# Kernel tuning notes

Measured on AMD Instinct MI355X. Metric: run time of the kernel, lower is better.

Reference implementation:

```python
import jax, jax.numpy as jnp
import numpy as np
import math

L, D, H, DK, DFF, B, S = 4, 512, 8, 256, 2048, 8, 256
HD = H * DK
EPS = 1e-6


def _norm(x, alpha, bias):
    # torch: alpha*(x-mean)/(std_unbiased + eps) + bias  (std uses ddof=1)
    mu = x.mean(axis=-1, keepdims=True)
    var = ((x - mu) ** 2).sum(axis=-1, keepdims=True) / (x.shape[-1] - 1)
    return alpha * (x - mu) / (jnp.sqrt(var) + EPS) + bias


def _positional_encoding():
    pos = jnp.arange(S, dtype=jnp.float32)[:, None]          # [S,1]
    i = jnp.arange(0, D, 2, dtype=jnp.float32)               # even indices
    pe_sin = jnp.sin(pos / (S ** (2.0 * i / D)))             # [S,D/2]
    pe_cos = jnp.cos(pos / (S ** (2.0 * (i + 1.0) / D)))     # [S,D/2]
    pe = jnp.zeros((S, D), dtype=jnp.float32)
    pe = pe.at[:, 0::2].set(pe_sin).at[:, 1::2].set(pe_cos)
    return pe


def setup_inputs() -> dict:
    key = jax.random.key(0)
    ks = jax.random.split(key, 16)
    sc = 0.02
    inp = {
        "data": jax.random.normal(ks[0], (B, S, D), dtype=jnp.float32),
        "attn_m": jax.random.randint(ks[1], (B, S), 0, 2, dtype=jnp.int32),
        "view_idx": 0,
        "seg_emb": jax.random.normal(ks[2], (3, D), dtype=jnp.float32) * sc,
        "Wq": jax.random.normal(ks[3], (L, D, HD), dtype=jnp.float32) * sc,
        "bq": jnp.zeros((L, HD), dtype=jnp.float32),
        "Wk": jax.random.normal(ks[4], (L, D, HD), dtype=jnp.float32) * sc,
        "bk": jnp.zeros((L, HD), dtype=jnp.float32),
        "Wv": jax.random.normal(ks[5], (L, D, HD), dtype=jnp.float32) * sc,
        "bv": jnp.zeros((L, HD), dtype=jnp.float32),
        "Wo": jax.random.normal(ks[6], (L, HD, D), dtype=jnp.float32) * sc,
        "bo": jnp.zeros((L, D), dtype=jnp.float32),
        "W1": jax.random.normal(ks[7], (L, D, DFF), dtype=jnp.float32) * sc,
        "b1": jnp.zeros((L, DFF), dtype=jnp.float32),
        "W2": jax.random.normal(ks[8], (L, DFF, D), dtype=jnp.float32) * sc,
        "b2": jnp.zeros((L, D), dtype=jnp.float32),
        "alpha1": jnp.ones((L, D), dtype=jnp.float32),
        "bias1": jnp.zeros((L, D), dtype=jnp.float32),
        "alpha2": jnp.ones((L, D), dtype=jnp.float32),
        "bias2": jnp.zeros((L, D), dtype=jnp.float32),
        "alpha_f": jnp.ones((D,), dtype=jnp.float32),
        "bias_f": jnp.zeros((D,), dtype=jnp.float32),
    }
    return inp


def reference(data, attn_m, view_idx, seg_emb, Wq, bq, Wk, bk, Wv, bv, Wo, bo,
              W1, b1, W2, b2, alpha1, bias1, alpha2, bias2, alpha_f, bias_f):
    # positional encoder: x*sqrt(d_f) + pe + seg_embedding(view_idx*seq_len)
    pe = _positional_encoding()
    seg_idx = view_idx * S  # scalar; must be < 3 (view_idx == 0 in practice)
    x = data * math.sqrt(D) + pe[None, :, :] + seg_emb[seg_idx][None, None, :]

    # mask: attn_m [B,S] -> [B,1,1,S] bool, True = masked (key axis)
    maskb = attn_m.astype(bool)[:, None, None, :]

    for i in range(L):
        x2 = _norm(x, alpha1[i], bias1[i])
        q = (x2 @ Wq[i] + bq[i]).reshape(B, S, H, DK).transpose(0, 2, 1, 3)
        k = (x2 @ Wk[i] + bk[i]).reshape(B, S, H, DK).transpose(0, 2, 1, 3)
        v = (x2 @ Wv[i] + bv[i]).reshape(B, S, H, DK).transpose(0, 2, 1, 3)
        scores = jnp.einsum('bhqd,bhkd->bhqk', q, k) / math.sqrt(DK)
        scores = jnp.where(maskb, -1e9, scores)
        attnw = jax.nn.softmax(scores, axis=-1)
        o = jnp.einsum('bhqk,bhkd->bhqd', attnw, v)
        o = o.transpose(0, 2, 1, 3).reshape(B, S, HD) @ Wo[i] + bo[i]
        x = x + o
        x2 = _norm(x, alpha2[i], bias2[i])
        ff = jax.nn.relu(x2 @ W1[i] + b1[i]) @ W2[i] + b2[i]
        x = x + ff

    return _norm(x, alpha_f, bias_f)
```

## Files before the change

kernel.cpp:

```cpp
#include <hip/hip_runtime.h>
#include <hip/hip_bf16.h>

#define LNUM 4
#define DIM  512
#define SS   256

typedef unsigned short ushort_t;
typedef __attribute__((ext_vector_type(8))) short bf16x8;
typedef __attribute__((ext_vector_type(4))) float f32x4;
typedef __attribute__((ext_vector_type(8))) unsigned short u16x8;

#define VWAIT(n) asm volatile("s_waitcnt vmcnt(" #n ")" ::: "memory")
__device__ __forceinline__ void bar() { __builtin_amdgcn_s_barrier(); }

__device__ __forceinline__ ushort_t f2b(float f) {
  union { float f; unsigned u; } x; x.f = f;
  unsigned r = x.u + 0x7FFFu + ((x.u >> 16) & 1u);
  return (ushort_t)(r >> 16);
}

__device__ __forceinline__ void gload16(const void* g, void* s) {
  __builtin_amdgcn_global_load_lds((const __attribute__((address_space(1))) void*)g,
                                   (__attribute__((address_space(3))) void*)s, 16, 0, 0);
}

template<int TM, int TN, int EPI>
__global__ __launch_bounds__(256, 2)
void gemm_bt(const ushort_t* __restrict__ A, const ushort_t* __restrict__ B,
             const float* __restrict__ bias, const float* __restrict__ bias2,
             const float* __restrict__ bias3,
             ushort_t* __restrict__ outB, ushort_t* __restrict__ outB2,
             ushort_t* __restrict__ outB3, float* __restrict__ outF,
             int K, int lda, int ldb, int ldc, int nkz, int relu)
{
  constexpr int CA = TM / 32, CB = TN / 32, SN = CA + CB;
  constexpr int WM = TM / 32, WN = TN / 32;
  __shared__ ushort_t As[3 * TM * 64];
  __shared__ ushort_t Bs[3 * TN * 64];
  const int tid = threadIdx.x, lane = tid & 63, wid = tid >> 6;
  const int wm = wid >> 1, wn = wid & 1;
  const int kz = blockIdx.z, Kz = K / nkz, k0 = kz * Kz, nt = Kz >> 6;

  const ushort_t* Ab = A + (long)blockIdx.y * TM * lda + k0;
  const ushort_t* Bb = B + (long)blockIdx.x * TN * ldb + k0;

  const ushort_t* srcA[CA]; ushort_t* ldsA[CA];
  const ushort_t* srcB[CB]; ushort_t* ldsB[CB];
#pragma unroll
  for (int c = 0; c < CA; ++c) {
    int off = c * 4096 + tid * 16;
    int row = off >> 7;
    int scol = ((off & 127) ^ ((row & 7) << 4)) >> 1;
    srcA[c] = Ab + (long)row * lda + scol;
    ldsA[c] = As + c * 2048 + wid * 512;
  }
#pragma unroll
  for (int c = 0; c < CB; ++c) {
    int off = c * 4096 + tid * 16;
    int row = off >> 7;
    int scol = ((off & 127) ^ ((row & 7) << 4)) >> 1;
    srcB[c] = Bb + (long)row * ldb + scol;
    ldsB[c] = Bs + c * 2048 + wid * 512;
  }

  f32x4 acc[WM][WN] = {};

  auto STAGE = [&](int buf, int t) {
#pragma unroll
    for (int c = 0; c < CA; ++c) gload16(srcA[c] + t * 64, ldsA[c] + buf * TM * 64);
#pragma unroll
    for (int c = 0; c < CB; ++c) gload16(srcB[c] + t * 64, ldsB[c] + buf * TN * 64);
  };

  STAGE(0, 0);
  STAGE(1, 1);
  for (int t = 0; t < nt; ++t) {
    if (t < nt - 1) { if constexpr (SN == 6) VWAIT(6); else VWAIT(4); }
    else VWAIT(0);
    bar();
    if (t + 2 < nt) STAGE((t + 2) % 3, t + 2);
    const int buf = t % 3;
#pragma unroll
    for (int ks = 0; ks < 2; ++ks) {
      const int kb = ks * 64 + ((lane >> 4) << 4);
      bf16x8 af[WM], bfr[WN];
#pragma unroll
      for (int f = 0; f < WM; ++f) {
        int ra = wm * (TM / 2) + f * 16 + (lane & 15);
        af[f] = *(const bf16x8*)((const char*)As + buf * TM * 128 + ra * 128 + (kb ^ ((ra & 7) << 4)));
      }
#pragma unroll
      for (int g = 0; g < WN; ++g) {
        int rb = wn * (TN / 2) + g * 16 + (lane & 15);
        bfr[g] = *(const bf16x8*)((const char*)Bs + buf * TN * 128 + rb * 128 + (kb ^ ((rb & 7) << 4)));
      }
      __builtin_amdgcn_s_setprio(1);
#pragma unroll
      for (int i = 0; i < WM; ++i)
#pragma unroll
        for (int j = 0; j < WN; ++j)
          acc[i][j] = __builtin_amdgcn_mfma_f32_16x16x32_bf16(af[i], bfr[j], acc[i][j], 0, 0, 0);
      __builtin_amdgcn_s_setprio(0);
    }
  }

  const int row0 = blockIdx.y * TM + wm * (TM / 2) + ((lane >> 4) << 2);
  int col0 = blockIdx.x * TN + wn * (TN / 2) + (lane & 15);
  const float* bsel = bias;
  ushort_t* osel = outB;
  int seg = 0;
  if (EPI == 3) {
    seg = (blockIdx.x * TN) >> 11;
    if (seg == 1) { bsel = bias2; osel = outB2; }
    else if (seg == 2) { bsel = bias3; }
    col0 -= seg * 2048;
  }

  if (EPI == 3 && seg == 2) {
    ushort_t* Vt = As;
    bar();
#pragma unroll
    for (int i = 0; i < WM; ++i)
#pragma unroll
      for (int j = 0; j < WN; ++j) {
        const int colL = wn * (TN / 2) + j * 16 + (lane & 15);
        const float bv = bsel[(col0 + j * 16) & 2047];
#pragma unroll
        for (int r = 0; r < 4; ++r) {
          const int rowL = wm * (TM / 2) + i * 16 + ((lane >> 4) << 2) + r;
          Vt[colL * 136 + rowL] = f2b(acc[i][j][r] + bv);
        }
      }
    bar();
    const int colvBase = blockIdx.x * TN - 4096;
    const int h = colvBase >> 8, dk0 = colvBase & 255;
    const int rowBase = blockIdx.y * TM;
    const int bh = ((rowBase >> 8) << 3) + h;
    const int s0 = rowBase & 255;
    const int dkl = tid >> 2, scc = (tid & 3) * 32;
    ushort_t* dst = outB3 + ((long)bh << 16) + (long)(dk0 + dkl) * 256 + s0 + scc;
#pragma unroll
    for (int m = 0; m < 4; ++m)
      *(u16x8*)(dst + m * 8) = *(const u16x8*)(Vt + dkl * 136 + scc + m * 8);
    return;
  }

#pragma unroll
  for (int i = 0; i < WM; ++i) {
#pragma unroll
    for (int j = 0; j < WN; ++j) {
      const int col = col0 + j * 16;
      float bv;
      if (EPI == 2) bv = (kz == 0) ? bias[col] : 0.f;
      else          bv = bsel[col];
#pragma unroll
      for (int r = 0; r < 4; ++r) {
        const int row = row0 + i * 16 + r;
        float v = acc[i][j][r] + bv;
        if (EPI == 2) {
          outF[(long)kz * 1048576 + (long)row * ldc + col] = v;
        } else {
          if (relu) v = fmaxf(v, 0.f);
          osel[(long)row * ldc + col] = f2b(v);
        }
      }
    }
  }
}

__global__ __launch_bounds__(256)
void attn_k(const ushort_t* __restrict__ qb, const ushort_t* __restrict__ kbf,
            const ushort_t* __restrict__ vT, const int* __restrict__ attnm,
            ushort_t* __restrict__ ao)
{
  __shared__ ushort_t Qs[64 * 256];
  __shared__ ushort_t KV[3][64 * 256];
  __shared__ int smask[256];
  const int qt = blockIdx.x, bh = blockIdx.y, b = bh >> 3, h = bh & 7;
  const int tid = threadIdx.x, lane = tid & 63, wid = tid >> 6;

  smask[tid] = attnm[b * 256 + tid];
  VWAIT(0);

  int srow[8], scol[8];
#pragma unroll
  for (int c = 0; c < 8; ++c) {
    int off = c * 4096 + tid * 16;
    srow[c] = off >> 9;
    scol[c] = ((off & 511) ^ ((srow[c] & 7) << 4)) >> 1;
  }

#define STQ() do { _Pragma("unroll") for (int c = 0; c < 8; ++c) \
  gload16(qb + (long)(b * 256 + qt * 64 + srow[c]) * 2048 + h * 256 + scol[c], Qs + c * 2048 + wid * 512); } while (0)
#define STK(KC, DST) do { _Pragma("unroll") for (int c = 0; c < 8; ++c) \
  gload16(kbf + (long)(b * 256 + (KC) * 64 + srow[c]) * 2048 + h * 256 + scol[c], (DST) + c * 2048 + wid * 512); } while (0)
#define STV(VC, DST) do { _Pragma("unroll") for (int c = 0; c < 8; ++c) \
  gload16(vT + ((long)bh << 16) + (long)((VC) * 64 + srow[c]) * 256 + scol[c], (DST) + c * 2048 + wid * 512); } while (0)

  f32x4 accs[16] = {};
  f32x4 acco[4][4] = {};

#define QKC(IDX, KVB) do { __builtin_amdgcn_s_setprio(1); _Pragma("unroll") \
  for (int ks = 0; ks < 8; ++ks) { \
    const int kb = ks * 64 + ((lane >> 4) << 4); \
    const int ra = wid * 16 + (lane & 15); \
    bf16x8 aq = *(const bf16x8*)((const char*)Qs + ra * 512 + (kb ^ ((ra & 7) << 4))); \
    _Pragma("unroll") \
    for (int j = 0; j < 4; ++j) { \
      const int rb = j * 16 + (lane & 15); \
      bf16x8 bk_ = *(const bf16x8*)((const char*)(KVB) + rb * 512 + (kb ^ ((rb & 7) << 4))); \
      accs[(IDX) * 4 + j] = __builtin_amdgcn_mfma_f32_16x16x32_bf16(aq, bk_, accs[(IDX) * 4 + j], 0, 0, 0); \
    } \
  } __builtin_amdgcn_s_setprio(0); } while (0)

#define PVC(VC, KVB) do { __builtin_amdgcn_s_setprio(1); _Pragma("unroll") \
  for (int ks = 0; ks < 8; ++ks) { \
    const int kb = ks * 64 + ((lane >> 4) << 4); \
    const int ra = wid * 16 + (lane & 15); \
    bf16x8 pa = *(const bf16x8*)((const char*)Qs + ra * 512 + (kb ^ ((ra & 7) << 4))); \
    _Pragma("unroll") \
    for (int j = 0; j < 4; ++j) { \
      const int rb = j * 16 + (lane & 15); \
      bf16x8 bv_ = *(const bf16x8*)((const char*)(KVB) + rb * 512 + (kb ^ ((rb & 7) << 4))); \
      acco[VC][j] = __builtin_amdgcn_mfma_f32_16x16x32_bf16(pa, bv_, acco[VC][j], 0, 0, 0); \
    } \
  } __builtin_amdgcn_s_setprio(0); } while (0)

  STQ(); STK(0, KV[0]); STK(1, KV[1]);

  VWAIT(16); bar(); STK(2, KV[2]); QKC(0, KV[0]);
  VWAIT(8);  bar(); STK(3, KV[0]); QKC(1, KV[1]);
  VWAIT(8);  bar(); STV(0, KV[1]); QKC(2, KV[2]);
  VWAIT(8);  bar(); STV(1, KV[2]); QKC(3, KV[0]);

  bar();
  STV(2, KV[0]);

  {
    float mr[4] = {-3e38f, -3e38f, -3e38f, -3e38f}, sr[4] = {};
#pragma unroll
    for (int jj = 0; jj < 16; ++jj) {
      int key = jj * 16 + (lane & 15);
      bool mk = smask[key] != 0;
#pragma unroll
      for (int r = 0; r < 4; ++r) {
        float s = mk ? -1e9f : accs[jj][r] * 0.0625f;
        accs[jj][r] = s;
        mr[r] = fmaxf(mr[r], s);
      }
    }
#pragma unroll
    for (int o = 1; o < 16; o <<= 1)
#pragma unroll
      for (int r = 0; r < 4; ++r) mr[r] = fmaxf(mr[r], __shfl_xor(mr[r], o, 64));
#pragma unroll
    for (int jj = 0; jj < 16; ++jj)
#pragma unroll
      for (int r = 0; r < 4; ++r) {
        float e = __expf(accs[jj][r] - mr[r]);
        accs[jj][r] = e;
        sr[r] += e;
      }
#pragma unroll
    for (int o = 1; o < 16; o <<= 1)
#pragma unroll
      for (int r = 0; r < 4; ++r) sr[r] += __shfl_xor(sr[r], o, 64);
#pragma unroll
    for (int r = 0; r < 4; ++r) sr[r] = 1.f / sr[r];
#pragma unroll
    for (int jj = 0; jj < 16; ++jj)
#pragma unroll
      for (int r = 0; r < 4; ++r) {
        int prow = wid * 16 + ((lane >> 4) << 2) + r;
        int cb = (jj * 16 + (lane & 15)) * 2;
        *(ushort_t*)((char*)Qs + prow * 512 + (cb ^ ((prow & 7) << 4))) = f2b(accs[jj][r] * sr[r]);
      }
  }

  VWAIT(16); bar();                 PVC(0, KV[1]);
  VWAIT(8);  bar(); STV(3, KV[1]); PVC(1, KV[2]);
  VWAIT(8);  bar();                 PVC(2, KV[0]);
  VWAIT(0);  bar();                 PVC(3, KV[1]);

#pragma unroll
  for (int vc = 0; vc < 4; ++vc)
#pragma unroll
    for (int j = 0; j < 4; ++j)
#pragma unroll
      for (int r = 0; r < 4; ++r) {
        int q = qt * 64 + wid * 16 + ((lane >> 4) << 2) + r;
        int dk = vc * 64 + j * 16 + (lane & 15);
        ao[(long)(b * 256 + q) * 2048 + h * 256 + dk] = f2b(acco[vc][j][r]);
      }
#undef STQ
#undef STK
#undef STV
#undef QKC
#undef PVC
}

__global__ __launch_bounds__(256)
void build_x(const float* __restrict__ data, const float* __restrict__ seg,
             const int* __restrict__ viewp, float* __restrict__ x)
{
  int i = blockIdx.x * 256 + threadIdx.x;
  int d = i & 511;
  int s = (i >> 9) & 255;
  float ang = (float)s * exp2f((float)d * -0.03125f);
  float pe = (d & 1) ? cosf(ang) : sinf(ang);
  int vrow = viewp[0] * SS;
  x[i] = data[i] * 22.627416997969522f + pe + seg[vrow * DIM + d];
}

__global__ __launch_bounds__(256)
void lnorm_k(const float* __restrict__ x, const float* __restrict__ parts, int np,
             float* __restrict__ xout,
             const float* __restrict__ alpha, const float* __restrict__ beta,
             ushort_t* __restrict__ outB, float* __restrict__ outF)
{
  const int row = blockIdx.x, tid = threadIdx.x;
  const long base = (long)row * DIM;
  float2 v = ((const float2*)(x + base))[tid];
  if (np) {
    for (int p = 0; p < np; ++p) {
      float2 a = ((const float2*)(parts + (long)p * 1048576 + base))[tid];
      v.x += a.x; v.y += a.y;
    }
    ((float2*)(xout + base))[tid] = v;
  }
  float s = v.x + v.y;
#pragma unroll
  for (int o = 32; o; o >>= 1) s += __shfl_xor(s, o, 64);
  __shared__ float rs[4], rq[4];
  if ((tid & 63) == 0) rs[tid >> 6] = s;
  __syncthreads();
  const float mu = (rs[0] + rs[1] + rs[2] + rs[3]) * (1.f / 512.f);
  const float dx = v.x - mu, dy = v.y - mu;
  float q = dx * dx + dy * dy;
#pragma unroll
  for (int o = 32; o; o >>= 1) q += __shfl_xor(q, o, 64);
  if ((tid & 63) == 0) rq[tid >> 6] = q;
  __syncthreads();
  const float var = (rq[0] + rq[1] + rq[2] + rq[3]) * (1.f / 511.f);
  const float rstd = 1.f / (sqrtf(var) + 1e-6f);
  const int d0 = tid * 2;
  const float o0 = alpha[d0] * dx * rstd + beta[d0];
  const float o1 = alpha[d0 + 1] * dy * rstd + beta[d0 + 1];
  if (outB) { outB[base + d0] = f2b(o0); outB[base + d0 + 1] = f2b(o1); }
  else      { outF[base + d0] = o0;      outF[base + d0 + 1] = o1; }
}

__global__ __launch_bounds__(256)
void wtrans(const float* __restrict__ in, ushort_t* __restrict__ out,
            int R, int C, long ozs)
{
  __shared__ float t[32][33];
  const int z = blockIdx.z;
  const long zi = (long)z * R * C, zo = (long)z * ozs;
  const int c0 = blockIdx.x * 32, r0 = blockIdx.y * 32;
  const int tx = threadIdx.x & 31, ty = threadIdx.x >> 5;
#pragma unroll
  for (int i = 0; i < 4; ++i) t[ty + i * 8][tx] = in[zi + (long)(r0 + ty + i * 8) * C + c0 + tx];
  __syncthreads();
#pragma unroll
  for (int i = 0; i < 4; ++i) out[zo + (long)(c0 + ty + i * 8) * R + r0 + tx] = f2b(t[tx][ty + i * 8]);
}

extern "C" void kernel_launch(void* const* d_in, const int* in_sizes, int n_in,
                              void* d_out, int out_size, void* d_ws, size_t ws_size,
                              hipStream_t stream)
{
  const float* data  = (const float*)d_in[0];
  const int*   attnm = (const int*)d_in[1];
  const int*   viewp = (const int*)d_in[2];
  const float* seg   = (const float*)d_in[3];
  const float* Wq    = (const float*)d_in[4];
  const float* bq    = (const float*)d_in[5];
  const float* Wk    = (const float*)d_in[6];
  const float* bk    = (const float*)d_in[7];
  const float* Wv    = (const float*)d_in[8];
  const float* bv    = (const float*)d_in[9];
  const float* Wo    = (const float*)d_in[10];
  const float* bo    = (const float*)d_in[11];
  const float* W1    = (const float*)d_in[12];
  const float* b1    = (const float*)d_in[13];
  const float* W2    = (const float*)d_in[14];
  const float* b2    = (const float*)d_in[15];
  const float* al1   = (const float*)d_in[16];
  const float* be1   = (const float*)d_in[17];
  const float* al2   = (const float*)d_in[18];
  const float* be2   = (const float*)d_in[19];
  const float* alf   = (const float*)d_in[20];
  const float* bef   = (const float*)d_in[21];

  char* w = (char*)d_ws;
  const size_t MB = 1024 * 1024;
  ushort_t* qkvW = (ushort_t*)(w + 0 * MB);
  ushort_t* WoT  = (ushort_t*)(w + 24 * MB);
  ushort_t* W1T  = (ushort_t*)(w + 32 * MB);
  ushort_t* W2T  = (ushort_t*)(w + 40 * MB);
  float*    x    = (float*)   (w + 48 * MB);
  ushort_t* x2   = (ushort_t*)(w + 52 * MB);
  ushort_t* qb   = (ushort_t*)(w + 54 * MB);
  ushort_t* kbf  = (ushort_t*)(w + 62 * MB);
  ushort_t* vT   = (ushort_t*)(w + 70 * MB);
  ushort_t* ao   = (ushort_t*)(w + 78 * MB);
  ushort_t* ffh  = (ushort_t*)(w + 86 * MB);
  float*    parts= (float*)   (w + 94 * MB);

  dim3 blk(256);
  const long QKV_L = 6144L * 512;
  wtrans<<<dim3(64, 16, 4), blk, 0, stream>>>(Wq, qkvW + 0 * 2048 * 512, 512, 2048, QKV_L);
  wtrans<<<dim3(64, 16, 4), blk, 0, stream>>>(Wk, qkvW + 1 * 2048 * 512, 512, 2048, QKV_L);
  wtrans<<<dim3(64, 16, 4), blk, 0, stream>>>(Wv, qkvW + 2 * 2048 * 512, 512, 2048, QKV_L);
  wtrans<<<dim3(16, 64, 4), blk, 0, stream>>>(Wo, WoT, 2048, 512, 512L * 2048);
  wtrans<<<dim3(64, 16, 4), blk, 0, stream>>>(W1, W1T, 512, 2048, 2048L * 512);
  wtrans<<<dim3(16, 64, 4), blk, 0, stream>>>(W2, W2T, 2048, 512, 512L * 2048);
  build_x<<<4096, blk, 0, stream>>>(data, seg, viewp, x);

  for (int i = 0; i < LNUM; ++i) {
    if (i == 0)
      lnorm_k<<<2048, blk, 0, stream>>>(x, nullptr, 0, nullptr, al1, be1, x2, nullptr);
    gemm_bt<128, 64, 3><<<dim3(96, 16, 1), blk, 0, stream>>>(
        x2, qkvW + (long)i * QKV_L, bq + i * 2048, bk + i * 2048, bv + i * 2048,
        qb, kbf, vT, nullptr, 512, 512, 512, 2048, 1, 0);
    attn_k<<<dim3(4, 64), blk, 0, stream>>>(qb, kbf, vT, attnm, ao);
    gemm_bt<64, 64, 2><<<dim3(8, 32, 4), blk, 0, stream>>>(
        ao, WoT + (long)i * 512 * 2048, bo + i * 512, nullptr, nullptr,
        nullptr, nullptr, nullptr, parts, 2048, 2048, 2048, 512, 4, 0);
    lnorm_k<<<2048, blk, 0, stream>>>(x, parts, 4, x, al2 + i * 512, be2 + i * 512, x2, nullptr);
    gemm_bt<128, 64, 0><<<dim3(32, 16, 1), blk, 0, stream>>>(
        x2, W1T + (long)i * 2048 * 512, b1 + i * 2048, nullptr, nullptr,
        ffh, nullptr, nullptr, nullptr, 512, 512, 512, 2048, 1, 1);
    gemm_bt<64, 64, 2><<<dim3(8, 32, 4), blk, 0, stream>>>(
        ffh, W2T + (long)i * 512 * 2048, b2 + i * 512, nullptr, nullptr,
        nullptr, nullptr, nullptr, parts, 2048, 2048, 2048, 512, 4, 0);
    if (i < LNUM - 1)
      lnorm_k<<<2048, blk, 0, stream>>>(x, parts, 4, x, al1 + (i + 1) * 512, be1 + (i + 1) * 512, x2, nullptr);
    else
      lnorm_k<<<2048, blk, 0, stream>>>(x, parts, 4, x, alf, bef, nullptr, (float*)d_out);
  }
}
```

Baseline: 451.9 us.

## Rewrite attention as single-wave blocks loading K/V fragments directly from global

```diff
diff --git a/kernel.cpp b/kernel.cpp
--- a/kernel.cpp
+++ b/kernel.cpp
@@ -168,135 +168,112 @@
   }
 }
 
-__global__ __launch_bounds__(256)
+__global__ __launch_bounds__(64, 2)
 void attn_k(const ushort_t* __restrict__ qb, const ushort_t* __restrict__ kbf,
             const ushort_t* __restrict__ vT, const int* __restrict__ attnm,
             ushort_t* __restrict__ ao)
 {
-  __shared__ ushort_t Qs[64 * 256];
-  __shared__ ushort_t KV[3][64 * 256];
-  __shared__ int smask[256];
+  __shared__ ushort_t Ps[16 * 256];
   const int qt = blockIdx.x, bh = blockIdx.y, b = bh >> 3, h = bh & 7;
-  const int tid = threadIdx.x, lane = tid & 63, wid = tid >> 6;
-
-  smask[tid] = attnm[b * 256 + tid];
-  VWAIT(0);
-
-  int srow[8], scol[8];
-#pragma unroll
-  for (int c = 0; c < 8; ++c) {
-    int off = c * 4096 + tid * 16;
-    srow[c] = off >> 9;
-    scol[c] = ((off & 511) ^ ((srow[c] & 7) << 4)) >> 1;
-  }
-
-#define STQ() do { _Pragma("unroll") for (int c = 0; c < 8; ++c) \
-  gload16(qb + (long)(b * 256 + qt * 64 + srow[c]) * 2048 + h * 256 + scol[c], Qs + c * 2048 + wid * 512); } while (0)
-#define STK(KC, DST) do { _Pragma("unroll") for (int c = 0; c < 8; ++c) \
-  gload16(kbf + (long)(b * 256 + (KC) * 64 + srow[c]) * 2048 + h * 256 + scol[c], (DST) + c * 2048 + wid * 512); } while (0)
-#define STV(VC, DST) do { _Pragma("unroll") for (int c = 0; c < 8; ++c) \
-  gload16(vT + ((long)bh << 16) + (long)((VC) * 64 + srow[c]) * 256 + scol[c], (DST) + c * 2048 + wid * 512); } while (0)
-
-  f32x4 accs[16] = {};
-  f32x4 acco[4][4] = {};
-
-#define QKC(IDX, KVB) do { __builtin_amdgcn_s_setprio(1); _Pragma("unroll") \
-  for (int ks = 0; ks < 8; ++ks) { \
-    const int kb = ks * 64 + ((lane >> 4) << 4); \
-    const int ra = wid * 16 + (lane & 15); \
-    bf16x8 aq = *(const bf16x8*)((const char*)Qs + ra * 512 + (kb ^ ((ra & 7) << 4))); \
-    _Pragma("unroll") \
-    for (int j = 0; j < 4; ++j) { \
-      const int rb = j * 16 + (lane & 15); \
-      bf16x8 bk_ = *(const bf16x8*)((const char*)(KVB) + rb * 512 + (kb ^ ((rb & 7) << 4))); \
-      accs[(IDX) * 4 + j] = __builtin_amdgcn_mfma_f32_16x16x32_bf16(aq, bk_, accs[(IDX) * 4 + j], 0, 0, 0); \
-    } \
-  } __builtin_amdgcn_s_setprio(0); } while (0)
-
-#define PVC(VC, KVB) do { __builtin_amdgcn_s_setprio(1); _Pragma("unroll") \
-  for (int ks = 0; ks < 8; ++ks) { \
-    const int kb = ks * 64 + ((lane >> 4) << 4); \
-    const int ra = wid * 16 + (lane & 15); \
-    bf16x8 pa = *(const bf16x8*)((const char*)Qs + ra * 512 + (kb ^ ((ra & 7) << 4))); \
-    _Pragma("unroll") \
-    for (int j = 0; j < 4; ++j) { \
-      const int rb = j * 16 + (lane & 15); \
-      bf16x8 bv_ = *(const bf16x8*)((const char*)(KVB) + rb * 512 + (kb ^ ((rb & 7) << 4))); \
-      acco[VC][j] = __builtin_amdgcn_mfma_f32_16x16x32_bf16(pa, bv_, acco[VC][j], 0, 0, 0); \
-    } \
-  } __builtin_amdgcn_s_setprio(0); } while (0)
-
-  STQ(); STK(0, KV[0]); STK(1, KV[1]);
-
-  VWAIT(16); bar(); STK(2, KV[2]); QKC(0, KV[0]);
-  VWAIT(8);  bar(); STK(3, KV[0]); QKC(1, KV[1]);
-  VWAIT(8);  bar(); STV(0, KV[1]); QKC(2, KV[2]);
-  VWAIT(8);  bar(); STV(1, KV[2]); QKC(3, KV[0]);
-
-  bar();
-  STV(2, KV[0]);
-
-  {
-    float mr[4] = {-3e38f, -3e38f, -3e38f, -3e38f}, sr[4] = {};
-#pragma unroll
-    for (int jj = 0; jj < 16; ++jj) {
-      int key = jj * 16 + (lane & 15);
-      bool mk = smask[key] != 0;
-#pragma unroll
-      for (int r = 0; r < 4; ++r) {
-        float s = mk ? -1e9f : accs[jj][r] * 0.0625f;
-        accs[jj][r] = s;
-        mr[r] = fmaxf(mr[r], s);
-      }
-    }
-#pragma unroll
-    for (int o = 1; o < 16; o <<= 1)
-#pragma unroll
-      for (int r = 0; r < 4; ++r) mr[r] = fmaxf(mr[r], __shfl_xor(mr[r], o, 64));
-#pragma unroll
-    for (int jj = 0; jj < 16; ++jj)
-#pragma unroll
-      for (int r = 0; r < 4; ++r) {
-        float e = __expf(accs[jj][r] - mr[r]);
-        accs[jj][r] = e;
-        sr[r] += e;
-      }
-#pragma unroll
-    for (int o = 1; o < 16; o <<= 1)
-#pragma unroll
-      for (int r = 0; r < 4; ++r) sr[r] += __shfl_xor(sr[r], o, 64);
-#pragma unroll
-    for (int r = 0; r < 4; ++r) sr[r] = 1.f / sr[r];
-#pragma unroll
-    for (int jj = 0; jj < 16; ++jj)
-#pragma unroll
-      for (int r = 0; r < 4; ++r) {
-        int prow = wid * 16 + ((lane >> 4) << 2) + r;
-        int cb = (jj * 16 + (lane & 15)) * 2;
-        *(ushort_t*)((char*)Qs + prow * 512 + (cb ^ ((prow & 7) << 4))) = f2b(accs[jj][r] * sr[r]);
-      }
-  }
-
-  VWAIT(16); bar();                 PVC(0, KV[1]);
-  VWAIT(8);  bar(); STV(3, KV[1]); PVC(1, KV[2]);
-  VWAIT(8);  bar();                 PVC(2, KV[0]);
-  VWAIT(0);  bar();                 PVC(3, KV[1]);
-
-#pragma unroll
-  for (int vc = 0; vc < 4; ++vc)
-#pragma unroll
-    for (int j = 0; j < 4; ++j)
-#pragma unroll
-      for (int r = 0; r < 4; ++r) {
-        int q = qt * 64 + wid * 16 + ((lane >> 4) << 2) + r;
-        int dk = vc * 64 + j * 16 + (lane & 15);
-        ao[(long)(b * 256 + q) * 2048 + h * 256 + dk] = f2b(acco[vc][j][r]);
-      }
-#undef STQ
-#undef STK
-#undef STV
-#undef QKC
-#undef PVC
+  const int lane = threadIdx.x;
+  const int l15 = lane & 15, l4 = lane >> 4;
+  const int q0 = qt * 16;
+
+  unsigned mbits = 0;
+#pragma unroll
+  for (int kt = 0; kt < 16; ++kt)
+    mbits |= (attnm[b * 256 + kt * 16 + l15] != 0 ? 1u : 0u) << kt;
+
+  const ushort_t* qp = qb + (long)(b * 256 + q0 + l15) * 2048 + h * 256 + l4 * 8;
+  bf16x8 qf[8];
+#pragma unroll
+  for (int ks = 0; ks < 8; ++ks) qf[ks] = *(const bf16x8*)(qp + ks * 32);
+
+  f32x4 sacc[16] = {};
+  const ushort_t* kp = kbf + (long)(b * 256 + l15) * 2048 + h * 256 + l4 * 8;
+#pragma unroll 2
+  for (int kt = 0; kt < 16; ++kt) {
+    bf16x8 kf[8];
+#pragma unroll
+    for (int ks = 0; ks < 8; ++ks)
+      kf[ks] = *(const bf16x8*)(kp + (long)kt * 16 * 2048 + ks * 32);
+#pragma unroll
+    for (int ks = 0; ks < 8; ++ks)
+      sacc[kt] = __builtin_amdgcn_mfma_f32_16x16x32_bf16(qf[ks], kf[ks], sacc[kt], 0, 0, 0);
+  }
+
+  float mr[4] = {-3e38f, -3e38f, -3e38f, -3e38f}, sr[4] = {};
+#pragma unroll
+  for (int kt = 0; kt < 16; ++kt) {
+    const bool mk = (mbits >> kt) & 1;
+#pragma unroll
+    for (int r = 0; r < 4; ++r) {
+      float s = mk ? -1e9f : sacc[kt][r] * 0.0625f;
+      sacc[kt][r] = s;
+      mr[r] = fmaxf(mr[r], s);
+    }
+  }
+#pragma unroll
+  for (int o = 1; o < 16; o <<= 1)
+#pragma unroll
+    for (int r = 0; r < 4; ++r) mr[r] = fmaxf(mr[r], __shfl_xor(mr[r], o, 16));
+#pragma unroll
+  for (int kt = 0; kt < 16; ++kt)
+#pragma unroll
+    for (int r = 0; r < 4; ++r) {
+      float e = __expf(sacc[kt][r] - mr[r]);
+      sacc[kt][r] = e;
+      sr[r] += e;
+    }
+#pragma unroll
+  for (int o = 1; o < 16; o <<= 1)
+#pragma unroll
+    for (int r = 0; r < 4; ++r) sr[r] += __shfl_xor(sr[r], o, 16);
+#pragma unroll
+  for (int r = 0; r < 4; ++r) sr[r] = 1.f / sr[r];
+
+#pragma unroll
+  for (int kt = 0; kt < 16; ++kt)
+#pragma unroll
+    for (int r = 0; r < 4; ++r) {
+      const int row = l4 * 4 + r;
+      *(ushort_t*)((char*)Ps + row * 512 + (((kt * 16 + l15) * 2) ^ ((row & 7) << 4))) =
+          f2b(sacc[kt][r] * sr[r]);
+    }
+
+  bf16x8 pf[8];
+#pragma unroll
+  for (int ks = 0; ks < 8; ++ks)
+    pf[ks] = *(const bf16x8*)((const char*)Ps + l15 * 512 + ((ks * 64 + l4 * 16) ^ ((l15 & 7) << 4)));
+
+  f32x4 oacc[16] = {};
+  const ushort_t* vp = vT + ((long)bh << 16) + (long)l15 * 256 + l4 * 8;
+#pragma unroll 2
+  for (int dt = 0; dt < 16; ++dt) {
+    bf16x8 vf[8];
+#pragma unroll
+    for (int ks = 0; ks < 8; ++ks)
+      vf[ks] = *(const bf16x8*)(vp + dt * 16 * 256 + ks * 32);
+#pragma unroll
+    for (int ks = 0; ks < 8; ++ks)
+      oacc[dt] = __builtin_amdgcn_mfma_f32_16x16x32_bf16(pf[ks], vf[ks], oacc[dt], 0, 0, 0);
+  }
+
+#pragma unroll
+  for (int dt = 0; dt < 16; ++dt)
+#pragma unroll
+    for (int r = 0; r < 4; ++r) {
+      const int row = l4 * 4 + r;
+      *(ushort_t*)((char*)Ps + row * 512 + (((dt * 16 + l15) * 2) ^ ((row & 7) << 4))) =
+          f2b(oacc[dt][r]);
+    }
+  ushort_t* dst = ao + (long)(b * 256 + q0 + l15) * 2048 + h * 256 + l4 * 64;
+#pragma unroll
+  for (int m = 0; m < 8; ++m) {
+    const int cbyte = l4 * 128 + m * 16;
+    u16x8 v = *(const u16x8*)((const char*)Ps + l15 * 512 + (cbyte ^ ((l15 & 7) << 4)));
+    *(u16x8*)(dst + m * 8) = v;
+  }
 }
 
 __global__ __launch_bounds__(256)
@@ -424,7 +401,7 @@
     gemm_bt<128, 64, 3><<<dim3(96, 16, 1), blk, 0, stream>>>(
         x2, qkvW + (long)i * QKV_L, bq + i * 2048, bk + i * 2048, bv + i * 2048,
         qb, kbf, vT, nullptr, 512, 512, 512, 2048, 1, 0);
-    attn_k<<<dim3(4, 64), blk, 0, stream>>>(qb, kbf, vT, attnm, ao);
+    attn_k<<<dim3(16, 64), dim3(64), 0, stream>>>(qb, kbf, vT, attnm, ao);
     gemm_bt<64, 64, 2><<<dim3(8, 32, 4), blk, 0, stream>>>(
         ao, WoT + (long)i * 512 * 2048, bo + i * 512, nullptr, nullptr,
         nullptr, nullptr, nullptr, parts, 2048, 2048, 2048, 512, 4, 0);
```

Measured after the change: 616.8 us. 36.5% more time.
